# Performance work log

Measured on AMD Instinct MI355X. Metric: run time of the kernel, lower is better.

The kernel has to match this reference:

```python
import jax, jax.numpy as jnp
import numpy as np

EPS = 1e-06
LOG_BIAS = 1.0  # config.fire_log_bias


def setup_inputs() -> dict:
    key = jax.random.key(0)
    ks = jax.random.split(key, 5)
    S, H, W = 2048, 12, 32
    x = jax.random.normal(ks[0], (1, S, 768), dtype=jnp.float32)
    w1 = jax.random.normal(ks[1], (W, 1), dtype=jnp.float32) * 0.5
    b1 = jax.random.normal(ks[2], (W,), dtype=jnp.float32) * 0.1
    w2 = jax.random.normal(ks[3], (H, W), dtype=jnp.float32) * 0.2
    b2 = jax.random.normal(ks[4], (H,), dtype=jnp.float32) * 0.1
    c = jnp.float32(0.1)            # fire_init_c, trainable
    L_multiplier = jnp.float32(1.0)  # trainable
    init_L = jnp.float32(512.0)      # non-trainable buffer
    return {"x": x, "w1": w1, "b1": b1, "w2": w2, "b2": b2,
            "c": c, "L_multiplier": L_multiplier, "init_L": init_L}


def reference(x, w1, b1, w2, b2, c, L_multiplier, init_L):
    S = x.shape[1]
    pos = jnp.arange(S, dtype=jnp.float32)
    rel = pos[:, None] - pos[None, :]                      # [S, S]
    abs_rel = jnp.abs(rel) + EPS
    threshold = jnp.abs(L_multiplier * init_L)
    pos_norm = jnp.maximum(pos, threshold)[:, None] + EPS  # [S, 1]
    log_rel = jnp.log(abs_rel * c + LOG_BIAS + EPS)        # [S, S]
    log_norm = jnp.log(jnp.abs(c * pos_norm) + LOG_BIAS + EPS)  # [S, 1]
    nd = log_rel / log_norm                                # [S, S]
    # tiny MLP: Linear(1,W) -> ReLU -> Linear(W,H)
    h = jax.nn.relu(nd[..., None] * w1[:, 0] + b1)         # [S, S, W]
    bias = jnp.einsum('stw,hw->hst', h, w2) + b2[:, None, None]  # [H, S, S]
    return bias[None]                                      # [1, H, S, S]
```

## Files before the change

### kernel.cpp

```cpp
#include <hip/hip_runtime.h>
#include <math.h>


#define SDIM 2048
#define WDIM 32
#define HDIM 12
#define NK 33
#define EPSF 1e-6f
#define LOGB 1.0f

#define WS_T 0
#define WS_AB 64
#define WS_TOTAL (64 + 2 * NK * HDIM)

__global__ __launch_bounds__(512) void fire_precompute(
    const float* __restrict__ w1, const float* __restrict__ b1,
    const float* __restrict__ w2, const float* __restrict__ b2,
    float* __restrict__ ws)
{
    __shared__ float traw[WDIM], w1s[WDIM], b1s[WDIM];
    __shared__ int rnk[WDIM], neg[WDIM];
    const int tid = threadIdx.x;

    if (tid < WDIM) {
        float a = w1[tid], b = b1[tid];
        w1s[tid] = a; b1s[tid] = b;
        float t; int isneg;
        if (a > 0.f)      { t = -b / a; isneg = 0; }
        else if (a < 0.f) { t = -b / a; isneg = 1; }
        else {
            t = (b > 0.f) ? -INFINITY : INFINITY; isneg = 0;
        }
        traw[tid] = t; neg[tid] = isneg;
    }
    __syncthreads();

    if (tid < WDIM) {
        float t = traw[tid];
        int r = 0;
        for (int v = 0; v < WDIM; ++v) {
            float tv = traw[v];
            if (tv < t || (tv == t && v < tid)) r++;
        }
        rnk[tid] = r;
        ws[WS_T + r] = t;
    } else if (tid < 64) {
        ws[WS_T + tid] = INFINITY;
    }
    __syncthreads();

    if (tid < NK * HDIM) {
        const int k = tid % NK;
        const int h = tid / NK;
        float a = 0.f, bb = 0.f;
        for (int w = 0; w < WDIM; ++w) {
            const bool active = neg[w] ? (rnk[w] >= k) : (rnk[w] < k);
            if (active) {
                float w2v = w2[h * WDIM + w];
                a  += w2v * w1s[w];
                bb += w2v * b1s[w];
            }
        }
        bb += b2[h];
        ws[WS_AB + (k * HDIM + h) * 2 + 0] = a;
        ws[WS_AB + (k * HDIM + h) * 2 + 1] = bb;
    }
}

__global__ __launch_bounds__(512) void fire_main(
    const float* __restrict__ ws,
    const float* __restrict__ cptr, const float* __restrict__ lmptr,
    const float* __restrict__ ilptr, float* __restrict__ out)
{
    __shared__ float sT[64];
    __shared__ float sAB[2 * NK * HDIM];
    const int tid = threadIdx.x;

    if (tid < 64) sT[tid] = ws[WS_T + tid];
    for (int idx = tid; idx < 2 * NK * HDIM; idx += 512) sAB[idx] = ws[WS_AB + idx];
    __syncthreads();

    const int i = blockIdx.x;
    const float c   = cptr[0];
    const float thr = fabsf(lmptr[0] * ilptr[0]);
    const float pn  = fmaxf((float)i, thr) + EPSF;
    const float inv_ln = 1.0f / logf(fabsf(c * pn) + LOGB + EPSF);

    const int j0 = tid * 4;
    float nd[4];
    int kk[4];
    #pragma unroll
    for (int e = 0; e < 4; ++e) {
        int j = j0 + e;
        int dd = i - j; if (dd < 0) dd = -dd;
        float ar = (float)dd + EPSF;
        float x  = fmaf(ar, c, LOGB + EPSF);
        float ndv = logf(x) * inv_ln;
        nd[e] = ndv;
        int k = 0;
        if (ndv > sT[k + 31]) k += 32;
        if (ndv > sT[k + 15]) k += 16;
        if (ndv > sT[k + 7])  k += 8;
        if (ndv > sT[k + 3])  k += 4;
        if (ndv > sT[k + 1])  k += 2;
        if (ndv > sT[k])      k += 1;
        kk[e] = k;
    }

    const size_t base = (size_t)i * SDIM + (size_t)j0;
    #pragma unroll
    for (int h = 0; h < HDIM; ++h) {
        float4 v;
        float* vp = &v.x;
        #pragma unroll
        for (int e = 0; e < 4; ++e) {
            int idx = (kk[e] * HDIM + h) * 2;
            vp[e] = fmaf(sAB[idx], nd[e], sAB[idx + 1]);
        }
        *(float4*)(out + (size_t)h * SDIM * SDIM + base) = v;
    }
}

extern "C" void kernel_launch(void* const* d_in, const int* in_sizes, int n_in,
                              void* d_out, int out_size, void* d_ws, size_t ws_size,
                              hipStream_t stream)
{
    const float* w1 = (const float*)d_in[1];
    const float* b1 = (const float*)d_in[2];
    const float* w2 = (const float*)d_in[3];
    const float* b2 = (const float*)d_in[4];
    const float* c  = (const float*)d_in[5];
    const float* lm = (const float*)d_in[6];
    const float* il = (const float*)d_in[7];
    float* ws  = (float*)d_ws;
    float* out = (float*)d_out;

    fire_precompute<<<1, 512, 0, stream>>>(w1, b1, w2, b2, ws);
    fire_main<<<SDIM, 512, 0, stream>>>(ws, c, lm, il, out);
}
```

Measured before the change: 217.1 us.

## Use nontemporal stores, register thresholds, fast log2, and split rows across blocks

The main kernel now uses 256-thread blocks, with two blocks per output row. The breakpoint thresholds are kept in registers and the segment index is found by a linear count instead of a shared-memory binary search. Output is written with nontemporal vector stores, the per-segment coefficients are read as 128-bit shared loads, and logf is replaced by the faster __log2f. The aim is to cut shared-memory traffic and instruction count in a kernel dominated by stores. The trade-offs are lower log precision and a change in tie handling at the thresholds (>= instead of >).

```diff
diff --git a/kernel.cpp b/kernel.cpp
--- a/kernel.cpp
+++ b/kernel.cpp
@@ -9,9 +9,10 @@
 #define EPSF 1e-6f
 #define LOGB 1.0f
 
+typedef float v4f __attribute__((ext_vector_type(4)));
+
 #define WS_T 0
 #define WS_AB 64
-#define WS_TOTAL (64 + 2 * NK * HDIM)
 
 __global__ __launch_bounds__(512) void fire_precompute(
     const float* __restrict__ w1, const float* __restrict__ b1,
@@ -62,62 +63,68 @@
             }
         }
         bb += b2[h];
-        ws[WS_AB + (k * HDIM + h) * 2 + 0] = a;
-        ws[WS_AB + (k * HDIM + h) * 2 + 1] = bb;
+        ws[WS_AB + k * (2 * HDIM) + h * 2 + 0] = a;
+        ws[WS_AB + k * (2 * HDIM) + h * 2 + 1] = bb;
     }
 }
 
-__global__ __launch_bounds__(512) void fire_main(
+__global__ __launch_bounds__(256) void fire_main(
     const float* __restrict__ ws,
     const float* __restrict__ cptr, const float* __restrict__ lmptr,
     const float* __restrict__ ilptr, float* __restrict__ out)
 {
-    __shared__ float sT[64];
     __shared__ float sAB[2 * NK * HDIM];
     const int tid = threadIdx.x;
 
-    if (tid < 64) sT[tid] = ws[WS_T + tid];
-    for (int idx = tid; idx < 2 * NK * HDIM; idx += 512) sAB[idx] = ws[WS_AB + idx];
-    __syncthreads();
+    for (int idx = tid; idx < 2 * NK * HDIM; idx += 256) sAB[idx] = ws[WS_AB + idx];
 
-    const int i = blockIdx.x;
+    float thr_t[WDIM];
+    #pragma unroll
+    for (int w = 0; w < WDIM; ++w) thr_t[w] = ws[WS_T + w];
+
+    const int i  = blockIdx.x >> 1;
+    const int j0 = ((blockIdx.x & 1) << 10) + tid * 4;
+
     const float c   = cptr[0];
     const float thr = fabsf(lmptr[0] * ilptr[0]);
     const float pn  = fmaxf((float)i, thr) + EPSF;
-    const float inv_ln = 1.0f / logf(fabsf(c * pn) + LOGB + EPSF);
+    const float inv_l2n = 1.0f / __log2f(fabsf(c * pn) + LOGB + EPSF);
 
-    const int j0 = tid * 4;
+    __syncthreads();
+
     float nd[4];
-    int kk[4];
+    int   kk[4];
     #pragma unroll
     for (int e = 0; e < 4; ++e) {
         int j = j0 + e;
         int dd = i - j; if (dd < 0) dd = -dd;
-        float ar = (float)dd + EPSF;
-        float x  = fmaf(ar, c, LOGB + EPSF);
-        float ndv = logf(x) * inv_ln;
+        float x = fmaf((float)dd + EPSF, c, LOGB + EPSF);
+        float ndv = __log2f(x) * inv_l2n;
         nd[e] = ndv;
         int k = 0;
-        if (ndv > sT[k + 31]) k += 32;
-        if (ndv > sT[k + 15]) k += 16;
-        if (ndv > sT[k + 7])  k += 8;
-        if (ndv > sT[k + 3])  k += 4;
-        if (ndv > sT[k + 1])  k += 2;
-        if (ndv > sT[k])      k += 1;
+        #pragma unroll
+        for (int w = 0; w < WDIM; ++w) k += (ndv >= thr_t[w]) ? 1 : 0;
         kk[e] = k;
+    }
+
+    float o[HDIM][4];
+    #pragma unroll
+    for (int e = 0; e < 4; ++e) {
+        const v4f* abp = (const v4f*)(sAB + kk[e] * (2 * HDIM));
+        const float ndv = nd[e];
+        #pragma unroll
+        for (int m = 0; m < HDIM / 2; ++m) {
+            v4f p = abp[m];
+            o[2 * m + 0][e] = fmaf(p.x, ndv, p.y);
+            o[2 * m + 1][e] = fmaf(p.z, ndv, p.w);
+        }
     }
 
     const size_t base = (size_t)i * SDIM + (size_t)j0;
     #pragma unroll
     for (int h = 0; h < HDIM; ++h) {
-        float4 v;
-        float* vp = &v.x;
-        #pragma unroll
-        for (int e = 0; e < 4; ++e) {
-            int idx = (kk[e] * HDIM + h) * 2;
-            vp[e] = fmaf(sAB[idx], nd[e], sAB[idx + 1]);
-        }
-        *(float4*)(out + (size_t)h * SDIM * SDIM + base) = v;
+        v4f v = { o[h][0], o[h][1], o[h][2], o[h][3] };
+        __builtin_nontemporal_store(v, (v4f*)(out + (size_t)h * SDIM * SDIM + base));
     }
 }
 
@@ -136,5 +143,5 @@
     float* out = (float*)d_out;
 
     fire_precompute<<<1, 512, 0, stream>>>(w1, b1, w2, b2, ws);
-    fire_main<<<SDIM, 512, 0, stream>>>(ws, c, lm, il, out);
+    fire_main<<<SDIM * 2, 256, 0, stream>>>(ws, c, lm, il, out);
 }
```

Measured after the change: 229.0 us. 5.4% more time.
